# Kernel tuning notes

Hardware: AMD Instinct MI355X
Metric: run time of the kernel (lower is better)

The kernel has to match this reference:

```python
import jax, jax.numpy as jnp
import numpy as np

N = 100000
E = 1600000
D = 64
NEG_SLOPE = 0.2


def setup_inputs() -> dict:
    key = jax.random.key(0)
    ks = jax.random.split(key, 16)
    inp = {}
    inp['x'] = jax.random.normal(ks[0], (N, D), dtype=jnp.float32)
    for i, name in enumerate(['edges_pos_out', 'edges_pos_in', 'edges_neg_out', 'edges_neg_in']):
        inp[name] = jax.random.randint(ks[1 + i], (2, E), 0, N, dtype=jnp.int64)
    s = 1.0 / np.sqrt(D)
    inp['gat_W'] = jax.random.normal(ks[5], (2, 4, D, D), dtype=jnp.float32) * s
    inp['gat_att_src'] = jax.random.normal(ks[6], (2, 4, D), dtype=jnp.float32) * s
    inp['gat_att_dst'] = jax.random.normal(ks[7], (2, 4, D), dtype=jnp.float32) * s
    inp['gat_bias'] = jnp.zeros((2, 4, D), dtype=jnp.float32)
    inp['mlp_W1'] = jax.random.normal(ks[8], (2, 5 * D, D), dtype=jnp.float32) * (1.0 / np.sqrt(5 * D))
    inp['mlp_b1'] = jnp.zeros((2, D), dtype=jnp.float32)
    inp['mlp_W2'] = jax.random.normal(ks[9], (2, D, D), dtype=jnp.float32) * s
    inp['mlp_b2'] = jnp.zeros((2, D), dtype=jnp.float32)
    return inp


def _gat(x, W, att_src, att_dst, bias, src, dst):
    # PyG GATConv, heads=1, add_self_loops=True
    n = x.shape[0]
    h = x @ W                                  # [N, D]
    a_src = h @ att_src                        # [N]
    a_dst = h @ att_dst                        # [N]
    loops = jnp.arange(n, dtype=src.dtype)
    s = jnp.concatenate([src, loops])
    d = jnp.concatenate([dst, loops])
    alpha = jax.nn.leaky_relu(a_src[s] + a_dst[d], NEG_SLOPE)   # [E+N]
    m = jax.ops.segment_max(alpha, d, num_segments=n)
    e = jnp.exp(alpha - m[d])
    z = jax.ops.segment_sum(e, d, num_segments=n)
    w = e / z[d]
    out = jax.ops.segment_sum(w[:, None] * h[s], d, num_segments=n)
    return out + bias


def _sdr_layer(x, edge_lists, W, a_s, a_d, b, W1, b1, W2, b2):
    feats = [x]
    for r, (src, dst) in enumerate(edge_lists):
        feats.append(_gat(x, W[r], a_s[r], a_d[r], b[r], src, dst))
    combined = jnp.concatenate(feats, axis=1)          # [N, 5D]
    hidden = jnp.tanh(combined @ W1 + b1)
    return hidden @ W2 + b2


def reference(x, edges_pos_out, edges_pos_in, edges_neg_out, edges_neg_in,
              gat_W, gat_att_src, gat_att_dst, gat_bias,
              mlp_W1, mlp_b1, mlp_W2, mlp_b2):
    edge_lists = [(e[0], e[1]) for e in
                  (edges_pos_out, edges_pos_in, edges_neg_out, edges_neg_in)]
    for l in range(gat_W.shape[0]):
        x = _sdr_layer(x, edge_lists, gat_W[l], gat_att_src[l], gat_att_dst[l],
                       gat_bias[l], mlp_W1[l], mlp_b1[l], mlp_W2[l], mlp_b2[l])
    return x
```

## Files before the change

### kernel.cpp

```cpp
#include <hip/hip_runtime.h>
#include <hip/hip_bf16.h>
#include <math.h>

#define D 64
#define NEG 0.2f
#define WPB 4
#define BLK 256
#define DPB 128
#define MAXNB 1024
#define CHUNK 16384
#define PCHUNK 8192

typedef __attribute__((ext_vector_type(8))) short bf8;
typedef __attribute__((ext_vector_type(4))) float f4;
typedef __attribute__((ext_vector_type(4))) int i4;

__device__ __forceinline__ float lrelu(float v) { return v > 0.f ? v : NEG * v; }

__device__ __forceinline__ unsigned short f2bf(float f) {
    unsigned u = __float_as_uint(f);
    u = (u + 0x7fffu + ((u >> 16) & 1u)) >> 16;
    return (unsigned short)u;
}
__device__ __forceinline__ bf8 ld_frag_g(const unsigned short* p) {
    i4 v = *(const i4*)p;
    return __builtin_bit_cast(bf8, v);
}

__device__ __forceinline__ const int* edge_ptr(const int* e0, const int* e1,
                                               const int* e2, const int* e3, int r)
{
    return (r == 0) ? e0 : (r == 1) ? e1 : (r == 2) ? e2 : e3;
}


__global__ __launch_bounds__(256) void k_bcount(
    const int* __restrict__ e0, const int* __restrict__ e1,
    const int* __restrict__ e2, const int* __restrict__ e3,
    int* __restrict__ bcnt, int E, int NB)
{
    int r = blockIdx.y;
    const int* dst = edge_ptr(e0, e1, e2, e3, r) + E;
    __shared__ int hist[MAXNB];
    for (int i = threadIdx.x; i < NB; i += 256) hist[i] = 0;
    __syncthreads();
    int base = blockIdx.x * CHUNK;
    int end = base + CHUNK < E ? base + CHUNK : E;
    for (int i = base + threadIdx.x; i < end; i += 256)
        atomicAdd(&hist[dst[i] >> 7], 1);
    __syncthreads();
    for (int i = threadIdx.x; i < NB; i += 256)
        if (hist[i]) atomicAdd(&bcnt[r * NB + i], hist[i]);
}

__global__ __launch_bounds__(1024) void k_bscan(
    const int* __restrict__ bcnt, int* __restrict__ boff,
    int* __restrict__ bcur, int* __restrict__ prefix, int E, int N, int NB)
{
    int r = blockIdx.y;
    __shared__ int sh[1024];
    int t = threadIdx.x;
    int v = (t < NB) ? bcnt[r * NB + t] : 0;
    sh[t] = v;
    __syncthreads();
    for (int off = 1; off < 1024; off <<= 1) {
        int add = (t >= off) ? sh[t - off] : 0;
        __syncthreads();
        sh[t] += add;
        __syncthreads();
    }
    if (t < NB) {
        int excl = sh[t] - v;
        boff[r * (NB + 1) + t] = excl;
        bcur[r * NB + t] = excl;
    }
    if (t == 0) {
        boff[r * (NB + 1) + NB] = E;
        prefix[(size_t)r * (N + 1) + N] = E;
    }
}

__global__ __launch_bounds__(256) void k_part(
    const int* __restrict__ e0, const int* __restrict__ e1,
    const int* __restrict__ e2, const int* __restrict__ e3,
    int* __restrict__ gcur, unsigned* __restrict__ staging, int E, int NB)
{
    __shared__ unsigned vals[PCHUNK];
    __shared__ unsigned short bkt[PCHUNK];
    __shared__ int hist[MAXNB];
    __shared__ int sbase[MAXNB];
    __shared__ int gdelta[MAXNB];
    __shared__ int ssum[256];
    int r = blockIdx.y;
    const int* ep = edge_ptr(e0, e1, e2, e3, r);
    const int* srcp = ep;
    const int* dstp = ep + E;
    int t = threadIdx.x;
    for (int j = t; j < MAXNB; j += 256) hist[j] = 0;
    __syncthreads();
    int begin = blockIdx.x * PCHUNK;
    int end = begin + PCHUNK < E ? begin + PCHUNK : E;
    int cnt = end - begin;
    for (int i = begin + t; i < end; i += 256)
        atomicAdd(&hist[dstp[i] >> 7], 1);
    __syncthreads();
    int h0 = hist[t * 4], h1 = hist[t * 4 + 1], h2 = hist[t * 4 + 2], h3 = hist[t * 4 + 3];
    int lsum = h0 + h1 + h2 + h3;
    ssum[t] = lsum;
    __syncthreads();
    for (int off = 1; off < 256; off <<= 1) {
        int a = (t >= off) ? ssum[t - off] : 0;
        __syncthreads();
        ssum[t] += a;
        __syncthreads();
    }
    int ex = ssum[t] - lsum;
    sbase[t * 4] = ex;
    sbase[t * 4 + 1] = ex + h0;
    sbase[t * 4 + 2] = ex + h0 + h1;
    sbase[t * 4 + 3] = ex + h0 + h1 + h2;
    __syncthreads();
    for (int j = t; j < NB; j += 256) {
        int c = hist[j];
        int gb = c ? atomicAdd(&gcur[r * NB + j], c) : 0;
        gdelta[j] = gb - sbase[j];
    }
    __syncthreads();
    for (int j = t; j < MAXNB; j += 256) hist[j] = 0;
    __syncthreads();
    for (int i = begin + t; i < end; i += 256) {
        int d = dstp[i];
        int s = srcp[i];
        int b = d >> 7;
        int rank = atomicAdd(&hist[b], 1);
        int p = sbase[b] + rank;
        vals[p] = ((unsigned)s << 7) | (unsigned)(d & 127);
        bkt[p] = (unsigned short)b;
    }
    __syncthreads();
    unsigned* stg = staging + (size_t)r * E;
    for (int p = t; p < cnt; p += 256)
        stg[p + gdelta[bkt[p]]] = vals[p];
}

__global__ __launch_bounds__(256) void k_place(
    const unsigned* __restrict__ staging, const int* __restrict__ boff,
    int* __restrict__ prefix, int* __restrict__ srcs, int N, int E, int NB)
{
    int r = blockIdx.y;
    int b = blockIdx.x;
    int t = threadIdx.x;
    __shared__ int lcount[DPB];
    __shared__ int ls[DPB];
    __shared__ int lcur[DPB];
    int gbase = boff[r * (NB + 1) + b];
    int bcnt = boff[r * (NB + 1) + b + 1] - gbase;
    if (t < DPB) lcount[t] = 0;
    __syncthreads();
    const unsigned* st = staging + (size_t)r * E + gbase;
    for (int i = t; i < bcnt; i += 256)
        atomicAdd(&lcount[st[i] & 127], 1);
    __syncthreads();
    if (t < DPB) ls[t] = lcount[t];
    __syncthreads();
    for (int off = 1; off < DPB; off <<= 1) {
        int add = (t < DPB && t >= off) ? ls[t - off] : 0;
        __syncthreads();
        if (t < DPB) ls[t] += add;
        __syncthreads();
    }
    int lo = b * DPB;
    if (t < DPB) {
        int excl = ls[t] - lcount[t];
        lcur[t] = excl;
        int d = lo + t;
        if (d < N) prefix[(size_t)r * (N + 1) + d] = gbase + excl;
    }
    __syncthreads();
    for (int i = t; i < bcnt; i += 256) {
        unsigned v = st[i];
        int pos = atomicAdd(&lcur[v & 127], 1);
        srcs[(size_t)r * E + gbase + pos] = (int)(v >> 7);
    }
}


__global__ __launch_bounds__(256) void k_xcast(
    const float* __restrict__ x, unsigned short* __restrict__ xb, int n4)
{
    int i = blockIdx.x * 256 + threadIdx.x;
    if (i < n4) {
        float4 v = ((const float4*)x)[i];
        ushort4 o;
        o.x = f2bf(v.x); o.y = f2bf(v.y); o.z = f2bf(v.z); o.w = f2bf(v.w);
        ((ushort4*)xb)[i] = o;
    }
}

__global__ __launch_bounds__(64) void k_pack(
    const float* __restrict__ gatW, const float* __restrict__ atS,
    const float* __restrict__ atD, const float* __restrict__ W1,
    const float* __restrict__ W2, unsigned short* __restrict__ WgP,
    unsigned short* __restrict__ W1P, unsigned short* __restrict__ W2P)
{
    int f = blockIdx.x;
    int L = threadIdx.x;
    int kg = L >> 4, c = L & 15;
    unsigned short vals[8];
    unsigned short* dst;
    if (f < 80) {
        int m = f / 10, rem = f % 10;
        int l = m / 4, r = m % 4;
        int kc = rem / 5, ct = rem % 5;
        const float* W = gatW + (size_t)(l * 4 + r) * D * D;
        if (ct < 4) {
#pragma unroll
            for (int j = 0; j < 8; j++) {
                int k = kc * 32 + kg * 8 + j;
                vals[j] = f2bf(W[k * D + ct * 16 + c]);
            }
        } else {
            const float* att = (c == 0) ? atS + (size_t)(l * 4 + r) * D
                                        : atD + (size_t)(l * 4 + r) * D;
#pragma unroll
            for (int j = 0; j < 8; j++) {
                int k = kc * 32 + kg * 8 + j;
                float s = 0.f;
                if (c < 2)
                    for (int cc = 0; cc < D; cc++) s += W[k * D + cc] * att[cc];
                vals[j] = f2bf(s);
            }
        }
        dst = WgP + ((size_t)f * 64 + L) * 8;
    } else if (f < 160) {
        int f2 = f - 80;
        int l = f2 / 40, rem = f2 % 40;
        int kc = rem / 4, ct = rem % 4;
        const float* W = W1 + (size_t)l * 5 * D * D;
#pragma unroll
        for (int j = 0; j < 8; j++) {
            int k = kc * 32 + kg * 8 + j;
            vals[j] = f2bf(W[k * D + ct * 16 + c]);
        }
        dst = W1P + ((size_t)f2 * 64 + L) * 8;
    } else {
        int f3 = f - 160;
        int l = f3 / 8, rem = f3 % 8;
        int kc = rem / 4, ct = rem % 4;
        const float* W = W2 + (size_t)l * D * D;
#pragma unroll
        for (int j = 0; j < 8; j++) {
            int k = kc * 32 + kg * 8 + j;
            vals[j] = f2bf(W[k * D + ct * 16 + c]);
        }
        dst = W2P + ((size_t)f3 * 64 + L) * 8;
    }
    i4 v = __builtin_bit_cast(i4, *(bf8*)vals);
    *(i4*)dst = v;
}


__device__ __forceinline__ void gemm_h_body(
    bf8 a0, bf8 a1, const unsigned short* __restrict__ WgPl,
    unsigned short* __restrict__ h, float* __restrict__ a_s,
    float* __restrict__ a_d, int n0, int kg, int lo, int L, int N)
{
#pragma unroll
    for (int r = 0; r < 4; r++) {
        const unsigned short* Wbase = WgPl + (size_t)r * 10 * 512;
#pragma unroll
        for (int ct = 0; ct < 5; ct++) {
            f4 acc = {0.f, 0.f, 0.f, 0.f};
            bf8 b0 = ld_frag_g(Wbase + (size_t)ct * 512 + (size_t)L * 8);
            bf8 b1 = ld_frag_g(Wbase + (size_t)(5 + ct) * 512 + (size_t)L * 8);
            acc = __builtin_amdgcn_mfma_f32_16x16x32_bf16(a0, b0, acc, 0, 0, 0);
            acc = __builtin_amdgcn_mfma_f32_16x16x32_bf16(a1, b1, acc, 0, 0, 0);
#pragma unroll
            for (int q = 0; q < 4; q++) {
                int node = n0 + kg * 4 + q;
                if (node < N) {
                    if (ct < 4)
                        h[((size_t)r * N + node) * D + ct * 16 + lo] = f2bf(acc[q]);
                    else if (lo == 0)
                        a_s[(size_t)r * N + node] = acc[q];
                    else if (lo == 1)
                        a_d[(size_t)r * N + node] = acc[q];
                }
            }
        }
    }
}

__global__ __launch_bounds__(BLK) void k_gemm_h(
    const unsigned short* __restrict__ xb, const unsigned short* __restrict__ WgPl,
    unsigned short* __restrict__ h, float* __restrict__ a_s,
    float* __restrict__ a_d, int N)
{
    int w = threadIdx.x >> 6, L = threadIdx.x & 63;
    int n0 = blockIdx.x * 64 + w * 16;
    int lo = L & 15, kg = L >> 4;
    int nA = n0 + lo; if (nA >= N) nA = N - 1;
    bf8 a0 = ld_frag_g(xb + (size_t)nA * D + kg * 8);
    bf8 a1 = ld_frag_g(xb + (size_t)nA * D + 32 + kg * 8);
    gemm_h_body(a0, a1, WgPl, h, a_s, a_d, n0, kg, lo, L, N);
}

__global__ __launch_bounds__(BLK) void k_agg(
    const unsigned short* __restrict__ h, const float* __restrict__ a_sall,
    const float* __restrict__ a_dall, const int* __restrict__ prefix,
    const int* __restrict__ srcsall, const float* __restrict__ gatB,
    unsigned short* __restrict__ g, int N, int E)
{
    __shared__ int2 pairs[WPB][64];
    int r = blockIdx.y;
    int w = threadIdx.x >> 6, lane = threadIdx.x & 63;
    int half = lane >> 5, fl = lane & 31;
    int d = (blockIdx.x * WPB + w) * 2 + half;
    if (d >= N) d = N - 1;

    const unsigned short* hr = h + (size_t)r * N * D;
    const float* a_src = a_sall + (size_t)r * N;
    const int* starts = prefix + (size_t)r * (N + 1);
    const int* srcs = srcsall + (size_t)r * E;

    int base = starts[d];
    int cnt = starts[d + 1] - base;
    float ad = a_dall[(size_t)r * N + d];

    float e_self = __expf(lrelu(a_src[d] + ad));
    float zpart = (fl == 0) ? e_self : 0.f;
    float accx, accy;
    {
        unsigned u = ((const unsigned*)(hr + (size_t)d * D))[fl];
        accx = e_self * __uint_as_float(u << 16);
        accy = e_self * __uint_as_float(u & 0xffff0000u);
    }

    int cntmax = max(cnt, __shfl_xor(cnt, 32));
    for (int c0 = 0; c0 < cntmax; c0 += 32) {
        int jj = c0 + fl;
        bool valid = jj < cnt;
        int s = valid ? srcs[base + jj] : 0;
        float e = valid ? __expf(lrelu(a_src[s] + ad)) : 0.f;
        zpart += e;
        pairs[w][lane] = make_int2(s * (int)(D * 2), __float_as_int(e));
        __threadfence_block();
        int lim = cntmax - c0; if (lim > 32) lim = 32;
        int rlim = (lim + 7) & ~7;
#pragma unroll 4
        for (int t = 0; t < rlim; t += 2) {
            i4 pv = *(const i4*)(&pairs[w][half * 32 + t]);
            unsigned uA = *(const unsigned*)((const char*)hr + pv.x + fl * 4);
            unsigned uB = *(const unsigned*)((const char*)hr + pv.z + fl * 4);
            float eA = __int_as_float(pv.y), eB = __int_as_float(pv.w);
            accx = fmaf(eA, __uint_as_float(uA << 16), accx);
            accy = fmaf(eA, __uint_as_float(uA & 0xffff0000u), accy);
            accx = fmaf(eB, __uint_as_float(uB << 16), accx);
            accy = fmaf(eB, __uint_as_float(uB & 0xffff0000u), accy);
        }
        __threadfence_block();
    }

    float z = zpart;
#pragma unroll
    for (int off = 16; off; off >>= 1) z += __shfl_xor(z, off);

    float rz = 1.f / z;
    float vlo = accx * rz + gatB[r * D + 2 * fl];
    float vhi = accy * rz + gatB[r * D + 2 * fl + 1];
    unsigned o = (unsigned)f2bf(vlo) | ((unsigned)f2bf(vhi) << 16);
    ((unsigned*)g)[((size_t)r * N + d) * 32 + fl] = o;
}

__global__ __launch_bounds__(BLK) void k_mlp(
    const unsigned short* __restrict__ xb, const unsigned short* __restrict__ g,
    const unsigned short* __restrict__ W1Pl, const float* __restrict__ b1l,
    const unsigned short* __restrict__ W2Pl, const float* __restrict__ b2l,
    void* __restrict__ outp, int N, int last,
    const unsigned short* __restrict__ WgPn, unsigned short* __restrict__ hn,
    float* __restrict__ a_sn, float* __restrict__ a_dn)
{
    __shared__ unsigned short sh[WPB][16 * 80];
    int w = threadIdx.x >> 6, L = threadIdx.x & 63;
    int n0 = blockIdx.x * 64 + w * 16;
    int lo = L & 15, kg = L >> 4;
    int nA = n0 + lo; if (nA >= N) nA = N - 1;

    f4 acc[4];
#pragma unroll
    for (int ct = 0; ct < 4; ct++) acc[ct] = (f4){0.f, 0.f, 0.f, 0.f};

#pragma unroll
    for (int p = 0; p < 5; p++) {
        const unsigned short* plane = (p == 0) ? xb : g + (size_t)(p - 1) * N * D;
#pragma unroll
        for (int kc2 = 0; kc2 < 2; kc2++) {
            bf8 a = ld_frag_g(plane + (size_t)nA * D + kc2 * 32 + kg * 8);
            int kc = p * 2 + kc2;
#pragma unroll
            for (int ct = 0; ct < 4; ct++) {
                bf8 b = ld_frag_g(W1Pl + ((size_t)(kc * 4 + ct) * 512 + (size_t)L * 8));
                acc[ct] = __builtin_amdgcn_mfma_f32_16x16x32_bf16(a, b, acc[ct], 0, 0, 0);
            }
        }
    }

    unsigned short* tile = &sh[w][0];
#pragma unroll
    for (int ct = 0; ct < 4; ct++) {
        float bb = b1l[ct * 16 + lo];
#pragma unroll
        for (int q = 0; q < 4; q++)
            tile[(kg * 4 + q) * 80 + ct * 16 + lo] = f2bf(tanhf(acc[ct][q] + bb));
    }
    __syncthreads();

    f4 o[4];
#pragma unroll
    for (int ct = 0; ct < 4; ct++) o[ct] = (f4){0.f, 0.f, 0.f, 0.f};
#pragma unroll
    for (int kc = 0; kc < 2; kc++) {
        const unsigned short* ap = tile + lo * 80 + kc * 32 + kg * 8;
        i4 av = *(const i4*)ap;
        bf8 a = __builtin_bit_cast(bf8, av);
#pragma unroll
        for (int ct = 0; ct < 4; ct++) {
            bf8 b = ld_frag_g(W2Pl + ((size_t)(kc * 4 + ct) * 512 + (size_t)L * 8));
            o[ct] = __builtin_amdgcn_mfma_f32_16x16x32_bf16(a, b, o[ct], 0, 0, 0);
        }
    }
    __syncthreads();
#pragma unroll
    for (int ct = 0; ct < 4; ct++) {
        float bb = b2l[ct * 16 + lo];
#pragma unroll
        for (int q = 0; q < 4; q++) {
            int node = n0 + kg * 4 + q;
            int col = ct * 16 + lo;
            float v = o[ct][q] + bb;
            if (node < N) {
                if (last) ((float*)outp)[(size_t)node * D + col] = v;
                else ((unsigned short*)outp)[(size_t)node * D + col] = f2bf(v);
            }
            if (!last) tile[(kg * 4 + q) * 80 + col] = f2bf(v);
        }
    }
    if (last) return;

    __syncthreads();
    bf8 a0, a1;
    {
        i4 v0 = *(const i4*)(tile + lo * 80 + kg * 8);
        i4 v1 = *(const i4*)(tile + lo * 80 + 32 + kg * 8);
        a0 = __builtin_bit_cast(bf8, v0);
        a1 = __builtin_bit_cast(bf8, v1);
    }
    gemm_h_body(a0, a1, WgPn, hn, a_sn, a_dn, n0, kg, lo, L, N);
}


extern "C" void kernel_launch(void* const* d_in, const int* in_sizes, int n_in,
                              void* d_out, int out_size, void* d_ws, size_t ws_size,
                              hipStream_t stream)
{
    const float* x    = (const float*)d_in[0];
    const int*   e0   = (const int*)d_in[1];
    const int*   e1   = (const int*)d_in[2];
    const int*   e2   = (const int*)d_in[3];
    const int*   e3   = (const int*)d_in[4];
    const float* gatW = (const float*)d_in[5];
    const float* atS  = (const float*)d_in[6];
    const float* atD  = (const float*)d_in[7];
    const float* gatB = (const float*)d_in[8];
    const float* W1   = (const float*)d_in[9];
    const float* b1   = (const float*)d_in[10];
    const float* W2   = (const float*)d_in[11];
    const float* b2   = (const float*)d_in[12];
    float* out = (float*)d_out;

    const int N = in_sizes[0] / D;
    const int E = in_sizes[1] / 2;
    const int NB = (N + DPB - 1) / DPB;

    size_t off = 0;
    auto alloc = [&](size_t bytes) { size_t o = off; off = (off + bytes + 255) & ~(size_t)255; return o; };
    unsigned short* xb    = (unsigned short*)((char*)d_ws + alloc((size_t)N * D * 2));
    unsigned short* xnext = (unsigned short*)((char*)d_ws + alloc((size_t)N * D * 2));
    unsigned short* h     = (unsigned short*)((char*)d_ws + alloc((size_t)4 * N * D * 2));
    unsigned short* g     = (unsigned short*)((char*)d_ws + alloc((size_t)4 * N * D * 2));
    unsigned* staging = (unsigned*)g;
    float* a_s   = (float*)((char*)d_ws + alloc((size_t)4 * N * 4));
    float* a_d   = (float*)((char*)d_ws + alloc((size_t)4 * N * 4));
    int* prefix  = (int*)((char*)d_ws + alloc((size_t)4 * (N + 1) * 4));
    int* srcs    = (int*)((char*)d_ws + alloc((size_t)4 * E * 4));
    int* bcnt    = (int*)((char*)d_ws + alloc((size_t)4 * NB * 4));
    int* boff    = (int*)((char*)d_ws + alloc((size_t)4 * (NB + 1) * 4));
    int* bcur    = (int*)((char*)d_ws + alloc((size_t)4 * NB * 4));
    unsigned short* WgP = (unsigned short*)((char*)d_ws + alloc((size_t)80 * 512 * 2));
    unsigned short* W1P = (unsigned short*)((char*)d_ws + alloc((size_t)80 * 512 * 2));
    unsigned short* W2P = (unsigned short*)((char*)d_ws + alloc((size_t)16 * 512 * 2));
    (void)ws_size;

    const int cntBlocks  = (E + CHUNK - 1) / CHUNK;
    const int partBlocks = (E + PCHUNK - 1) / PCHUNK;
    const int tileBlocks = (N + 63) / 64;
    const int aggBlocks  = (N + 7) / 8;

    k_pack<<<176, 64, 0, stream>>>(gatW, atS, atD, W1, W2, WgP, W1P, W2P);
    k_xcast<<<(N * D / 4 + 255) / 256, 256, 0, stream>>>(x, xb, N * D / 4);

    hipMemsetAsync(bcnt, 0, (size_t)4 * NB * 4, stream);
    k_bcount<<<dim3(cntBlocks, 4), 256, 0, stream>>>(e0, e1, e2, e3, bcnt, E, NB);
    k_bscan<<<dim3(1, 4), 1024, 0, stream>>>(bcnt, boff, bcur, prefix, E, N, NB);
    k_part<<<dim3(partBlocks, 4), 256, 0, stream>>>(e0, e1, e2, e3, bcur, staging, E, NB);
    k_place<<<dim3(NB, 4), 256, 0, stream>>>(staging, boff, prefix, srcs, N, E, NB);

    k_gemm_h<<<tileBlocks, BLK, 0, stream>>>(xb, WgP, h, a_s, a_d, N);
    k_agg<<<dim3(aggBlocks, 4), BLK, 0, stream>>>(
        h, a_s, a_d, prefix, srcs, gatB, g, N, E);
    k_mlp<<<tileBlocks, BLK, 0, stream>>>(
        xb, g, W1P, b1, W2P, b2, xnext, N, 0,
        WgP + (size_t)40 * 512, h, a_s, a_d);

    k_agg<<<dim3(aggBlocks, 4), BLK, 0, stream>>>(
        h, a_s, a_d, prefix, srcs, gatB + (size_t)4 * D, g, N, E);
    k_mlp<<<tileBlocks, BLK, 0, stream>>>(
        xnext, g, W1P + (size_t)40 * 512, b1 + D, W2P + (size_t)8 * 512, b2 + D,
        out, N, 1, nullptr, nullptr, nullptr, nullptr);
}
```

Baseline: 594.5 us.

## Fuse per-bucket CSR placement into aggregation kernel and use bf16 dot2 accumulation

Removes the k_place kernel and the global prefix/srcs CSR arrays. Each k_agg block now handles one 128-destination bucket, counting-sorts that bucket's edges into shared memory (ECAP=4096 entries) and then aggregates 32 destinations per wave. Edge weights are packed to bf16 pairs and accumulated with the fdot2 bf16 builtin when available. This trades one kernel launch and a global write/read of sorted sources for a local sort that is redone in both layers, lower-precision attention weights, and a hard cap of 4096 edges per bucket with no bounds check.

After: 626.5 us. 5.4% more time.

```diff
diff --git a/kernel.cpp b/kernel.cpp
--- a/kernel.cpp
+++ b/kernel.cpp
@@ -10,10 +10,24 @@
 #define MAXNB 1024
 #define CHUNK 16384
 #define PCHUNK 8192
+#define ECAP 4096
 
 typedef __attribute__((ext_vector_type(8))) short bf8;
 typedef __attribute__((ext_vector_type(4))) float f4;
 typedef __attribute__((ext_vector_type(4))) int i4;
+
+#if defined(__has_builtin)
+#  if __has_builtin(__builtin_amdgcn_fdot2_f32_bf16) && __has_builtin(__builtin_amdgcn_perm)
+#    define HAS_BFDOT2 1
+#  endif
+#endif
+#ifndef HAS_BFDOT2
+#  define HAS_BFDOT2 0
+#endif
+
+#if HAS_BFDOT2
+typedef __bf16 bfv2 __attribute__((ext_vector_type(2)));
+#endif
 
 __device__ __forceinline__ float lrelu(float v) { return v > 0.f ? v : NEG * v; }
 
@@ -55,7 +69,7 @@
 
 __global__ __launch_bounds__(1024) void k_bscan(
     const int* __restrict__ bcnt, int* __restrict__ boff,
-    int* __restrict__ bcur, int* __restrict__ prefix, int E, int N, int NB)
+    int* __restrict__ bcur, int E, int NB)
 {
     int r = blockIdx.y;
     __shared__ int sh[1024];
@@ -74,16 +88,13 @@
         boff[r * (NB + 1) + t] = excl;
         bcur[r * NB + t] = excl;
     }
-    if (t == 0) {
-        boff[r * (NB + 1) + NB] = E;
-        prefix[(size_t)r * (N + 1) + N] = E;
-    }
+    if (t == 0) boff[r * (NB + 1) + NB] = E;
 }
 
 __global__ __launch_bounds__(256) void k_part(
     const int* __restrict__ e0, const int* __restrict__ e1,
     const int* __restrict__ e2, const int* __restrict__ e3,
-    int* __restrict__ gcur, unsigned* __restrict__ staging, int E, int NB)
+    int* __restrict__ gcur, unsigned* __restrict__ edges, int E, int NB)
 {
     __shared__ unsigned vals[PCHUNK];
     __shared__ unsigned short bkt[PCHUNK];
@@ -138,50 +149,9 @@
         bkt[p] = (unsigned short)b;
     }
     __syncthreads();
-    unsigned* stg = staging + (size_t)r * E;
+    unsigned* stg = edges + (size_t)r * E;
     for (int p = t; p < cnt; p += 256)
         stg[p + gdelta[bkt[p]]] = vals[p];
-}
-
-__global__ __launch_bounds__(256) void k_place(
-    const unsigned* __restrict__ staging, const int* __restrict__ boff,
-    int* __restrict__ prefix, int* __restrict__ srcs, int N, int E, int NB)
-{
-    int r = blockIdx.y;
-    int b = blockIdx.x;
-    int t = threadIdx.x;
-    __shared__ int lcount[DPB];
-    __shared__ int ls[DPB];
-    __shared__ int lcur[DPB];
-    int gbase = boff[r * (NB + 1) + b];
-    int bcnt = boff[r * (NB + 1) + b + 1] - gbase;
-    if (t < DPB) lcount[t] = 0;
-    __syncthreads();
-    const unsigned* st = staging + (size_t)r * E + gbase;
-    for (int i = t; i < bcnt; i += 256)
-        atomicAdd(&lcount[st[i] & 127], 1);
-    __syncthreads();
-    if (t < DPB) ls[t] = lcount[t];
-    __syncthreads();
-    for (int off = 1; off < DPB; off <<= 1) {
-        int add = (t < DPB && t >= off) ? ls[t - off] : 0;
-        __syncthreads();
-        if (t < DPB) ls[t] += add;
-        __syncthreads();
-    }
-    int lo = b * DPB;
-    if (t < DPB) {
-        int excl = ls[t] - lcount[t];
-        lcur[t] = excl;
-        int d = lo + t;
-        if (d < N) prefix[(size_t)r * (N + 1) + d] = gbase + excl;
-    }
-    __syncthreads();
-    for (int i = t; i < bcnt; i += 256) {
-        unsigned v = st[i];
-        int pos = atomicAdd(&lcur[v & 127], 1);
-        srcs[(size_t)r * E + gbase + pos] = (int)(v >> 7);
-    }
 }
 
 
@@ -307,69 +277,135 @@
 
 __global__ __launch_bounds__(BLK) void k_agg(
     const unsigned short* __restrict__ h, const float* __restrict__ a_sall,
-    const float* __restrict__ a_dall, const int* __restrict__ prefix,
-    const int* __restrict__ srcsall, const float* __restrict__ gatB,
-    unsigned short* __restrict__ g, int N, int E)
-{
-    __shared__ int2 pairs[WPB][64];
+    const float* __restrict__ a_dall, const int* __restrict__ boff,
+    const unsigned* __restrict__ edges, const float* __restrict__ gatB,
+    unsigned short* __restrict__ g, int N, int E, int NB)
+{
+    __shared__ int sorted[ECAP];
+    __shared__ int lcount[DPB];
+    __shared__ int lstart[DPB];
+    __shared__ int lcur[DPB];
+    __shared__ float adst[DPB];
+    __shared__ i4 comb[WPB][32];
     int r = blockIdx.y;
-    int w = threadIdx.x >> 6, lane = threadIdx.x & 63;
+    int bktb = blockIdx.x;
+    int t = threadIdx.x;
+    int w = t >> 6, lane = t & 63;
     int half = lane >> 5, fl = lane & 31;
-    int d = (blockIdx.x * WPB + w) * 2 + half;
-    if (d >= N) d = N - 1;
+    int d0 = bktb * DPB;
 
     const unsigned short* hr = h + (size_t)r * N * D;
-    const float* a_src = a_sall + (size_t)r * N;
-    const int* starts = prefix + (size_t)r * (N + 1);
-    const int* srcs = srcsall + (size_t)r * E;
-
-    int base = starts[d];
-    int cnt = starts[d + 1] - base;
-    float ad = a_dall[(size_t)r * N + d];
-
-    float e_self = __expf(lrelu(a_src[d] + ad));
-    float zpart = (fl == 0) ? e_self : 0.f;
-    float accx, accy;
-    {
-        unsigned u = ((const unsigned*)(hr + (size_t)d * D))[fl];
-        accx = e_self * __uint_as_float(u << 16);
-        accy = e_self * __uint_as_float(u & 0xffff0000u);
-    }
-
-    int cntmax = max(cnt, __shfl_xor(cnt, 32));
-    for (int c0 = 0; c0 < cntmax; c0 += 32) {
-        int jj = c0 + fl;
-        bool valid = jj < cnt;
-        int s = valid ? srcs[base + jj] : 0;
-        float e = valid ? __expf(lrelu(a_src[s] + ad)) : 0.f;
-        zpart += e;
-        pairs[w][lane] = make_int2(s * (int)(D * 2), __float_as_int(e));
-        __threadfence_block();
-        int lim = cntmax - c0; if (lim > 32) lim = 32;
-        int rlim = (lim + 7) & ~7;
+    const float* asr = a_sall + (size_t)r * N;
+
+    int base = boff[r * (NB + 1) + bktb];
+    int cnt  = boff[r * (NB + 1) + bktb + 1] - base;
+    const unsigned* eb = edges + (size_t)r * E + base;
+
+    if (t < DPB) {
+        lcount[t] = 0;
+        int dd = d0 + t;
+        adst[t] = (dd < N) ? a_dall[(size_t)r * N + dd] : 0.f;
+    }
+    __syncthreads();
+    for (int i = t; i < cnt; i += 256)
+        atomicAdd(&lcount[eb[i] & 127], 1);
+    __syncthreads();
+    if (t < DPB) lstart[t] = lcount[t];
+    __syncthreads();
+    for (int off = 1; off < DPB; off <<= 1) {
+        int add = (t < DPB && t >= off) ? lstart[t - off] : 0;
+        __syncthreads();
+        if (t < DPB) lstart[t] += add;
+        __syncthreads();
+    }
+    if (t < DPB) {
+        int excl = lstart[t] - lcount[t];
+        lstart[t] = excl;
+        lcur[t] = excl;
+    }
+    __syncthreads();
+    for (int i = t; i < cnt; i += 256) {
+        unsigned v = eb[i];
+        int pos = atomicAdd(&lcur[v & 127], 1);
+        sorted[pos] = (int)(v >> 7);
+    }
+    __syncthreads();
+
+    const float gb0 = gatB[r * D + 2 * fl];
+    const float gb1 = gatB[r * D + 2 * fl + 1];
+
+    for (int p = 0; p < 16; p++) {
+        int dl = w * 32 + p * 2 + half;
+        int d  = d0 + dl;
+        bool real = d < N;
+        int dd = real ? d : d0;
+        int cd = lcount[dl];
+        int st = lstart[dl];
+        float ad = adst[dl];
+
+        float e_self = __expf(lrelu(asr[dd] + ad));
+        float zpart = (fl == 0) ? e_self : 0.f;
+        float accx, accy;
+        {
+            unsigned u = ((const unsigned*)(hr + (size_t)dd * D))[fl];
+            accx = e_self * __uint_as_float(u << 16);
+            accy = e_self * __uint_as_float(u & 0xffff0000u);
+        }
+
+        int cmax = max(cd, __shfl_xor(cd, 32));
+        for (int c0 = 0; c0 < cmax; c0 += 32) {
+            int jj = c0 + fl;
+            bool valid = jj < cd;
+            int src = valid ? sorted[st + jj] : 0;
+            float e = valid ? __expf(lrelu(asr[src] + ad)) : 0.f;
+            zpart += e;
+            int q = fl >> 1;
+            ((int*)&comb[w][half * 16 + q])[fl & 1] = src * (int)(D * 2);
+            float eo = __shfl_down(e, 1);
+            if ((fl & 1) == 0) {
+                unsigned pk = (unsigned)f2bf(e) | ((unsigned)f2bf(eo) << 16);
+                ((int*)&comb[w][half * 16 + q])[2] = (int)pk;
+            }
+            __threadfence_block();
+            int lim = cmax - c0; if (lim > 32) lim = 32;
+            int steps = (lim + 1) >> 1;
 #pragma unroll 4
-        for (int t = 0; t < rlim; t += 2) {
-            i4 pv = *(const i4*)(&pairs[w][half * 32 + t]);
-            unsigned uA = *(const unsigned*)((const char*)hr + pv.x + fl * 4);
-            unsigned uB = *(const unsigned*)((const char*)hr + pv.z + fl * 4);
-            float eA = __int_as_float(pv.y), eB = __int_as_float(pv.w);
-            accx = fmaf(eA, __uint_as_float(uA << 16), accx);
-            accy = fmaf(eA, __uint_as_float(uA & 0xffff0000u), accy);
-            accx = fmaf(eB, __uint_as_float(uB << 16), accx);
-            accy = fmaf(eB, __uint_as_float(uB & 0xffff0000u), accy);
-        }
-        __threadfence_block();
-    }
-
-    float z = zpart;
-#pragma unroll
-    for (int off = 16; off; off >>= 1) z += __shfl_xor(z, off);
-
-    float rz = 1.f / z;
-    float vlo = accx * rz + gatB[r * D + 2 * fl];
-    float vhi = accy * rz + gatB[r * D + 2 * fl + 1];
-    unsigned o = (unsigned)f2bf(vlo) | ((unsigned)f2bf(vhi) << 16);
-    ((unsigned*)g)[((size_t)r * N + d) * 32 + fl] = o;
+            for (int s = 0; s < steps; s++) {
+                i4 pv = comb[w][half * 16 + s];
+                unsigned uA = *(const unsigned*)((const char*)hr + pv.x + fl * 4);
+                unsigned uB = *(const unsigned*)((const char*)hr + pv.y + fl * 4);
+#if HAS_BFDOT2
+                unsigned lopk = __builtin_amdgcn_perm(uB, uA, 0x05040100u);
+                unsigned hipk = __builtin_amdgcn_perm(uB, uA, 0x07060302u);
+                bfv2 ep2 = __builtin_bit_cast(bfv2, (unsigned)pv.z);
+                accx = __builtin_amdgcn_fdot2_f32_bf16(
+                    __builtin_bit_cast(bfv2, lopk), ep2, accx, false);
+                accy = __builtin_amdgcn_fdot2_f32_bf16(
+                    __builtin_bit_cast(bfv2, hipk), ep2, accy, false);
+#else
+                float eA = __uint_as_float(((unsigned)pv.z) << 16);
+                float eB = __uint_as_float(((unsigned)pv.z) & 0xffff0000u);
+                accx = fmaf(eA, __uint_as_float(uA << 16), accx);
+                accy = fmaf(eA, __uint_as_float(uA & 0xffff0000u), accy);
+                accx = fmaf(eB, __uint_as_float(uB << 16), accx);
+                accy = fmaf(eB, __uint_as_float(uB & 0xffff0000u), accy);
+#endif
+            }
+            __threadfence_block();
+        }
+
+        float z = zpart;
+#pragma unroll
+        for (int off = 16; off; off >>= 1) z += __shfl_xor(z, off);
+
+        if (real) {
+            float rz = 1.f / z;
+            float vlo = accx * rz + gb0;
+            float vhi = accy * rz + gb1;
+            unsigned o = (unsigned)f2bf(vlo) | ((unsigned)f2bf(vhi) << 16);
+            ((unsigned*)g)[((size_t)r * N + d) * 32 + fl] = o;
+        }
+    }
 }
 
 __global__ __launch_bounds__(BLK) void k_mlp(
@@ -488,11 +524,9 @@
     unsigned short* xnext = (unsigned short*)((char*)d_ws + alloc((size_t)N * D * 2));
     unsigned short* h     = (unsigned short*)((char*)d_ws + alloc((size_t)4 * N * D * 2));
     unsigned short* g     = (unsigned short*)((char*)d_ws + alloc((size_t)4 * N * D * 2));
-    unsigned* staging = (unsigned*)g;
+    unsigned* edges = (unsigned*)((char*)d_ws + alloc((size_t)4 * E * 4));
     float* a_s   = (float*)((char*)d_ws + alloc((size_t)4 * N * 4));
     float* a_d   = (float*)((char*)d_ws + alloc((size_t)4 * N * 4));
-    int* prefix  = (int*)((char*)d_ws + alloc((size_t)4 * (N + 1) * 4));
-    int* srcs    = (int*)((char*)d_ws + alloc((size_t)4 * E * 4));
     int* bcnt    = (int*)((char*)d_ws + alloc((size_t)4 * NB * 4));
     int* boff    = (int*)((char*)d_ws + alloc((size_t)4 * (NB + 1) * 4));
     int* bcur    = (int*)((char*)d_ws + alloc((size_t)4 * NB * 4));
@@ -504,26 +538,24 @@
     const int cntBlocks  = (E + CHUNK - 1) / CHUNK;
     const int partBlocks = (E + PCHUNK - 1) / PCHUNK;
     const int tileBlocks = (N + 63) / 64;
-    const int aggBlocks  = (N + 7) / 8;
 
     k_pack<<<176, 64, 0, stream>>>(gatW, atS, atD, W1, W2, WgP, W1P, W2P);
     k_xcast<<<(N * D / 4 + 255) / 256, 256, 0, stream>>>(x, xb, N * D / 4);
 
     hipMemsetAsync(bcnt, 0, (size_t)4 * NB * 4, stream);
     k_bcount<<<dim3(cntBlocks, 4), 256, 0, stream>>>(e0, e1, e2, e3, bcnt, E, NB);
-    k_bscan<<<dim3(1, 4), 1024, 0, stream>>>(bcnt, boff, bcur, prefix, E, N, NB);
-    k_part<<<dim3(partBlocks, 4), 256, 0, stream>>>(e0, e1, e2, e3, bcur, staging, E, NB);
-    k_place<<<dim3(NB, 4), 256, 0, stream>>>(staging, boff, prefix, srcs, N, E, NB);
+    k_bscan<<<dim3(1, 4), 1024, 0, stream>>>(bcnt, boff, bcur, E, NB);
+    k_part<<<dim3(partBlocks, 4), 256, 0, stream>>>(e0, e1, e2, e3, bcur, edges, E, NB);
 
     k_gemm_h<<<tileBlocks, BLK, 0, stream>>>(xb, WgP, h, a_s, a_d, N);
-    k_agg<<<dim3(aggBlocks, 4), BLK, 0, stream>>>(
-        h, a_s, a_d, prefix, srcs, gatB, g, N, E);
+    k_agg<<<dim3(NB, 4), BLK, 0, stream>>>(
+        h, a_s, a_d, boff, edges, gatB, g, N, E, NB);
     k_mlp<<<tileBlocks, BLK, 0, stream>>>(
         xb, g, W1P, b1, W2P, b2, xnext, N, 0,
         WgP + (size_t)40 * 512, h, a_s, a_d);
 
-    k_agg<<<dim3(aggBlocks, 4), BLK, 0, stream>>>(
-        h, a_s, a_d, prefix, srcs, gatB + (size_t)4 * D, g, N, E);
+    k_agg<<<dim3(NB, 4), BLK, 0, stream>>>(
+        h, a_s, a_d, boff, edges, gatB + (size_t)4 * D, g, N, E, NB);
     k_mlp<<<tileBlocks, BLK, 0, stream>>>(
         xnext, g, W1P + (size_t)40 * 512, b1 + D, W2P + (size_t)8 * 512, b2 + D,
         out, N, 1, nullptr, nullptr, nullptr, nullptr);
```
